# Kernel tuning notes

Hardware: AMD Instinct MI355X
Metric: run time of the kernel (lower is better)

Reference implementation:

```python
import jax, jax.numpy as jnp
import numpy as np


def setup_inputs() -> dict:
    key = jax.random.key(0)
    k1, k2 = jax.random.split(key)
    B, N, C = 2, 1024, 64  # batch_size, block_num, out_channels
    regional_means = jax.random.normal(k1, (B, N, C), dtype=jnp.float32)
    # nn.Parameter randn then kaiming_uniform_: just use scaled random weights
    W = jax.random.normal(k2, (C, C), dtype=jnp.float32) * (1.0 / np.sqrt(C))
    return {"regional_means": regional_means, "W": W, "c": C}


def reference(regional_means, W, c):
    # regional_means: (B, N, c); W: (c, c)
    B, N, _ = regional_means.shape
    M = W @ W.T  # (c, c), PSD Mahalanobis metric
    # pairwise differences diff[b, i, j] = means[b, i] - means[b, j]  -> (B, N, N, c)
    # (original materializes this via repeat/permute; sign flip from its final
    #  permute is irrelevant since the quadratic form is even)
    diff = regional_means[:, :, None, :] - regional_means[:, None, :, :]
    # quadratic form q[b,i,j] = diff^T M diff
    q = jnp.einsum('bijc,cd,bijd->bij', diff, M, diff)
    adj = jnp.exp(-q) + jnp.eye(N, dtype=regional_means.dtype)[None, :, :]
    return adj
```

## Files before the change

kernel.cpp:

```cpp
#include <hip/hip_runtime.h>
#include <math.h>


__global__ void __launch_bounds__(256) compute_Y_kernel(
    const float* __restrict__ X, const float* __restrict__ W,
    float* __restrict__ Y, float* __restrict__ r)
{
    __shared__ float Ws[64][64];
    __shared__ float Xs[4][64];

    const int t = threadIdx.x;

    const float4* W4 = (const float4*)W;
    float4* Ws4 = (float4*)&Ws[0][0];
#pragma unroll
    for (int c = 0; c < 4; ++c) Ws4[c * 256 + t] = W4[c * 256 + t];

    const int row0 = blockIdx.x * 4;
    const int rr = t >> 6;
    const int lane = t & 63;
    Xs[rr][lane] = X[(row0 + rr) * 64 + lane];
    __syncthreads();

    float y = 0.f;
#pragma unroll
    for (int k = 0; k < 64; ++k)
        y = fmaf(Xs[rr][k], Ws[k][lane], y);

    Y[(row0 + rr) * 64 + lane] = y;

    float s = y * y;
#pragma unroll
    for (int off = 32; off > 0; off >>= 1) s += __shfl_down(s, off, 64);
    if (lane == 0) r[row0 + rr] = s;
}

__global__ void __launch_bounds__(256) adj_tile_kernel(
    const float* __restrict__ Y, const float* __restrict__ r,
    float* __restrict__ out, int N)
{
    __shared__ float Yi[64][65];
    __shared__ float Yj[64][65];

    const int b  = blockIdx.z;
    const int ib = blockIdx.y * 64;
    const int jb = blockIdx.x * 64;
    const float* __restrict__ Yb = Y + (size_t)b * N * 64;
    const float* __restrict__ rb = r + (size_t)b * N;
    const int t = threadIdx.x;

#pragma unroll
    for (int c = 0; c < 16; ++c) {
        int idx = c * 256 + t;
        int row = idx >> 6, col = idx & 63;
        Yi[row][col] = Yb[(size_t)(ib + row) * 64 + col];
        Yj[row][col] = Yb[(size_t)(jb + row) * 64 + col];
    }
    __syncthreads();

    const int tj = t & 15;
    const int ti = t >> 4;
    const int i0 = ti * 4, j0 = tj * 4;

    float acc[4][4] = {};
#pragma unroll 4
    for (int k = 0; k < 64; ++k) {
        float a0 = Yi[i0 + 0][k], a1 = Yi[i0 + 1][k],
              a2 = Yi[i0 + 2][k], a3 = Yi[i0 + 3][k];
        float b0 = Yj[j0 + 0][k], b1 = Yj[j0 + 1][k],
              b2 = Yj[j0 + 2][k], b3 = Yj[j0 + 3][k];
        acc[0][0] = fmaf(a0, b0, acc[0][0]); acc[0][1] = fmaf(a0, b1, acc[0][1]);
        acc[0][2] = fmaf(a0, b2, acc[0][2]); acc[0][3] = fmaf(a0, b3, acc[0][3]);
        acc[1][0] = fmaf(a1, b0, acc[1][0]); acc[1][1] = fmaf(a1, b1, acc[1][1]);
        acc[1][2] = fmaf(a1, b2, acc[1][2]); acc[1][3] = fmaf(a1, b3, acc[1][3]);
        acc[2][0] = fmaf(a2, b0, acc[2][0]); acc[2][1] = fmaf(a2, b1, acc[2][1]);
        acc[2][2] = fmaf(a2, b2, acc[2][2]); acc[2][3] = fmaf(a2, b3, acc[2][3]);
        acc[3][0] = fmaf(a3, b0, acc[3][0]); acc[3][1] = fmaf(a3, b1, acc[3][1]);
        acc[3][2] = fmaf(a3, b2, acc[3][2]); acc[3][3] = fmaf(a3, b3, acc[3][3]);
    }

    float ri[4], rj[4];
#pragma unroll
    for (int ii = 0; ii < 4; ++ii) ri[ii] = rb[ib + i0 + ii];
#pragma unroll
    for (int jj = 0; jj < 4; ++jj) rj[jj] = rb[jb + j0 + jj];

    const size_t base = (size_t)b * N * N;
#pragma unroll
    for (int ii = 0; ii < 4; ++ii) {
        const int gi = ib + i0 + ii;
        float4 v;
#pragma unroll
        for (int jj = 0; jj < 4; ++jj) {
            const int gj = jb + j0 + jj;
            float q = ri[ii] + rj[jj] - 2.f * acc[ii][jj];
            float val = __expf(-q);
            if (gi == gj) val += 1.f;
            (&v.x)[jj] = val;
        }
        ((float4*)(out + base + (size_t)gi * N + jb))[tj] = v;
    }
}

extern "C" void kernel_launch(void* const* d_in, const int* in_sizes, int n_in,
                              void* d_out, int out_size, void* d_ws, size_t ws_size,
                              hipStream_t stream) {
    const float* X = (const float*)d_in[0];
    const float* W = (const float*)d_in[1];
    float* out = (float*)d_out;

    const int C  = 64;
    const int BN = in_sizes[0] / C;
    const int N  = (int)(((long long)out_size * C) / in_sizes[0]);
    const int B  = BN / N;

    float* Y = (float*)d_ws;
    float* r = Y + (size_t)BN * C;

    compute_Y_kernel<<<BN / 4, 256, 0, stream>>>(X, W, Y, r);
    adj_tile_kernel<<<dim3(N / 64, N / 64, B), 256, 0, stream>>>(Y, r, out, N);
}
```

Baseline: 68.24 us.

## Fuse Y=XW projection into adjacency tile kernel, recomputing per tile

Removes the separate projection kernel and workspace round-trip. Each 64x64 output tile block now loads W and its X rows into shared memory, computes Y for the i and j blocks, takes the row norms from them, and then runs the Gram product using transposed shared layouts read as float4. Diagonal tiles reuse Yi instead of computing Yj. This drops one launch and the global-memory traffic for Y and r. In exchange every tile redundantly recomputes the projection and uses more shared memory (about 70KB per block), which limits occupancy.

```diff
diff --git a/kernel.cpp b/kernel.cpp
--- a/kernel.cpp
+++ b/kernel.cpp
@@ -2,88 +2,114 @@
 #include <math.h>
 
 
-__global__ void __launch_bounds__(256) compute_Y_kernel(
+#define PAD 68
+
+__global__ void __launch_bounds__(256, 2) adj_fused_kernel(
     const float* __restrict__ X, const float* __restrict__ W,
-    float* __restrict__ Y, float* __restrict__ r)
-{
-    __shared__ float Ws[64][64];
-    __shared__ float Xs[4][64];
-
-    const int t = threadIdx.x;
-
-    const float4* W4 = (const float4*)W;
-    float4* Ws4 = (float4*)&Ws[0][0];
-#pragma unroll
-    for (int c = 0; c < 4; ++c) Ws4[c * 256 + t] = W4[c * 256 + t];
-
-    const int row0 = blockIdx.x * 4;
-    const int rr = t >> 6;
-    const int lane = t & 63;
-    Xs[rr][lane] = X[(row0 + rr) * 64 + lane];
-    __syncthreads();
-
-    float y = 0.f;
-#pragma unroll
-    for (int k = 0; k < 64; ++k)
-        y = fmaf(Xs[rr][k], Ws[k][lane], y);
-
-    Y[(row0 + rr) * 64 + lane] = y;
-
-    float s = y * y;
-#pragma unroll
-    for (int off = 32; off > 0; off >>= 1) s += __shfl_down(s, off, 64);
-    if (lane == 0) r[row0 + rr] = s;
-}
-
-__global__ void __launch_bounds__(256) adj_tile_kernel(
-    const float* __restrict__ Y, const float* __restrict__ r,
     float* __restrict__ out, int N)
 {
-    __shared__ float Yi[64][65];
-    __shared__ float Yj[64][65];
+    __shared__ float Ws [64][PAD];
+    __shared__ float Xs [64][PAD];
+    __shared__ float Yit[64][PAD];
+    __shared__ float Yjt[64][PAD];
+    __shared__ float ris[64], rjs[64];
 
     const int b  = blockIdx.z;
     const int ib = blockIdx.y * 64;
     const int jb = blockIdx.x * 64;
-    const float* __restrict__ Yb = Y + (size_t)b * N * 64;
-    const float* __restrict__ rb = r + (size_t)b * N;
-    const int t = threadIdx.x;
+    const bool samet = (ib == jb);
+    const int t  = threadIdx.x;
+    const int tr = t >> 4;
+    const int tc = t & 15;
+    const int r0 = tr * 4, c0 = tc * 4;
 
+    const float* __restrict__ Xb = X + ((size_t)b * N) * 64;
+
+    const float4* W4  = (const float4*)W;
+    const float4* Xi4 = (const float4*)(Xb + (size_t)ib * 64);
 #pragma unroll
-    for (int c = 0; c < 16; ++c) {
+    for (int c = 0; c < 4; ++c) {
         int idx = c * 256 + t;
-        int row = idx >> 6, col = idx & 63;
-        Yi[row][col] = Yb[(size_t)(ib + row) * 64 + col];
-        Yj[row][col] = Yb[(size_t)(jb + row) * 64 + col];
+        int row = idx >> 4;
+        int col = (idx & 15) * 4;
+        *(float4*)&Ws[row][col] = W4[idx];
+        *(float4*)&Xs[row][col] = Xi4[idx];
     }
     __syncthreads();
 
-    const int tj = t & 15;
-    const int ti = t >> 4;
-    const int i0 = ti * 4, j0 = tj * 4;
+    auto computeY = [&](float (*Yt)[PAD]) {
+        float y[4][4] = {};
+#pragma unroll 4
+        for (int k4 = 0; k4 < 64; k4 += 4) {
+            float4 xv[4], wv[4];
+#pragma unroll
+            for (int rr = 0; rr < 4; ++rr) xv[rr] = *(const float4*)&Xs[r0 + rr][k4];
+#pragma unroll
+            for (int kk = 0; kk < 4; ++kk) wv[kk] = *(const float4*)&Ws[k4 + kk][c0];
+#pragma unroll
+            for (int rr = 0; rr < 4; ++rr)
+#pragma unroll
+                for (int kk = 0; kk < 4; ++kk) {
+                    float x = (&xv[rr].x)[kk];
+#pragma unroll
+                    for (int cc = 0; cc < 4; ++cc)
+                        y[rr][cc] = fmaf(x, (&wv[kk].x)[cc], y[rr][cc]);
+                }
+        }
+#pragma unroll
+        for (int cc = 0; cc < 4; ++cc)
+            *(float4*)&Yt[c0 + cc][r0] =
+                make_float4(y[0][cc], y[1][cc], y[2][cc], y[3][cc]);
+    };
 
+    computeY(Yit);
+    __syncthreads();
+
+    float (*Yjp)[PAD] = Yit;
+    if (!samet) {
+        const float4* Xj4 = (const float4*)(Xb + (size_t)jb * 64);
+#pragma unroll
+        for (int c = 0; c < 4; ++c) {
+            int idx = c * 256 + t;
+            *(float4*)&Xs[idx >> 4][(idx & 15) * 4] = Xj4[idx];
+        }
+        __syncthreads();
+        computeY(Yjt);
+        Yjp = Yjt;
+        __syncthreads();
+    }
+
+    if (t < 128) {
+        const int i = t & 63;
+        float (*Yp)[PAD] = (t < 64) ? Yit : Yjp;
+        float s = 0.f;
+#pragma unroll 8
+        for (int c = 0; c < 64; ++c) { float v = Yp[c][i]; s = fmaf(v, v, s); }
+        if (t < 64) ris[i] = s; else rjs[i] = s;
+    }
+    __syncthreads();
+
+    const int i0 = r0, j0 = c0;
     float acc[4][4] = {};
-#pragma unroll 4
+#pragma unroll 8
     for (int k = 0; k < 64; ++k) {
-        float a0 = Yi[i0 + 0][k], a1 = Yi[i0 + 1][k],
-              a2 = Yi[i0 + 2][k], a3 = Yi[i0 + 3][k];
-        float b0 = Yj[j0 + 0][k], b1 = Yj[j0 + 1][k],
-              b2 = Yj[j0 + 2][k], b3 = Yj[j0 + 3][k];
-        acc[0][0] = fmaf(a0, b0, acc[0][0]); acc[0][1] = fmaf(a0, b1, acc[0][1]);
-        acc[0][2] = fmaf(a0, b2, acc[0][2]); acc[0][3] = fmaf(a0, b3, acc[0][3]);
-        acc[1][0] = fmaf(a1, b0, acc[1][0]); acc[1][1] = fmaf(a1, b1, acc[1][1]);
-        acc[1][2] = fmaf(a1, b2, acc[1][2]); acc[1][3] = fmaf(a1, b3, acc[1][3]);
-        acc[2][0] = fmaf(a2, b0, acc[2][0]); acc[2][1] = fmaf(a2, b1, acc[2][1]);
-        acc[2][2] = fmaf(a2, b2, acc[2][2]); acc[2][3] = fmaf(a2, b3, acc[2][3]);
-        acc[3][0] = fmaf(a3, b0, acc[3][0]); acc[3][1] = fmaf(a3, b1, acc[3][1]);
-        acc[3][2] = fmaf(a3, b2, acc[3][2]); acc[3][3] = fmaf(a3, b3, acc[3][3]);
+        float4 a  = *(const float4*)&Yit[k][i0];
+        float4 bb = *(const float4*)&Yjp[k][j0];
+        acc[0][0] = fmaf(a.x, bb.x, acc[0][0]); acc[0][1] = fmaf(a.x, bb.y, acc[0][1]);
+        acc[0][2] = fmaf(a.x, bb.z, acc[0][2]); acc[0][3] = fmaf(a.x, bb.w, acc[0][3]);
+        acc[1][0] = fmaf(a.y, bb.x, acc[1][0]); acc[1][1] = fmaf(a.y, bb.y, acc[1][1]);
+        acc[1][2] = fmaf(a.y, bb.z, acc[1][2]); acc[1][3] = fmaf(a.y, bb.w, acc[1][3]);
+        acc[2][0] = fmaf(a.z, bb.x, acc[2][0]); acc[2][1] = fmaf(a.z, bb.y, acc[2][1]);
+        acc[2][2] = fmaf(a.z, bb.z, acc[2][2]); acc[2][3] = fmaf(a.z, bb.w, acc[2][3]);
+        acc[3][0] = fmaf(a.w, bb.x, acc[3][0]); acc[3][1] = fmaf(a.w, bb.y, acc[3][1]);
+        acc[3][2] = fmaf(a.w, bb.z, acc[3][2]); acc[3][3] = fmaf(a.w, bb.w, acc[3][3]);
     }
 
     float ri[4], rj[4];
 #pragma unroll
-    for (int ii = 0; ii < 4; ++ii) ri[ii] = rb[ib + i0 + ii];
+    for (int ii = 0; ii < 4; ++ii) ri[ii] = ris[i0 + ii];
 #pragma unroll
-    for (int jj = 0; jj < 4; ++jj) rj[jj] = rb[jb + j0 + jj];
+    for (int jj = 0; jj < 4; ++jj) rj[jj] = rjs[j0 + jj];
 
     const size_t base = (size_t)b * N * N;
 #pragma unroll
@@ -98,7 +124,7 @@
             if (gi == gj) val += 1.f;
             (&v.x)[jj] = val;
         }
-        ((float4*)(out + base + (size_t)gi * N + jb))[tj] = v;
+        ((float4*)(out + base + (size_t)gi * N + jb))[tc] = v;
     }
 }
 
@@ -114,9 +140,5 @@
     const int N  = (int)(((long long)out_size * C) / in_sizes[0]);
     const int B  = BN / N;
 
-    float* Y = (float*)d_ws;
-    float* r = Y + (size_t)BN * C;
-
-    compute_Y_kernel<<<BN / 4, 256, 0, stream>>>(X, W, Y, r);
-    adj_tile_kernel<<<dim3(N / 64, N / 64, B), 256, 0, stream>>>(Y, r, out, N);
+    adj_fused_kernel<<<dim3(N / 64, N / 64, B), 256, 0, stream>>>(X, W, out, N);
 }
```

Result: slower. 72.54 us (+6.3%).

## Compute Gram matrix with bf16 MFMA per-wave 16x16 tiles instead of FP32 FMA

Applied to the files above, without the earlier changes.

Stores the projected Y in bf16 and computes each 16x16 block of the pairwise Gram matrix with two 16x16x32 bf16 MFMA instructions per wave, reading operands straight from global memory with no shared-memory staging. The squared norms are taken from the bf16-rounded values so they stay consistent with the dot products. The goal is to remove the FP32 FMA inner loop and the LDS tile loads. In exchange, Y loses precision, which can noticeably perturb exp(-q) for large norms. Output stores become scalar and strided per lane rather than float4 writes.

```diff
diff --git a/kernel.cpp b/kernel.cpp
--- a/kernel.cpp
+++ b/kernel.cpp
@@ -1,16 +1,19 @@
 #include <hip/hip_runtime.h>
+#include <hip/hip_bf16.h>
 #include <math.h>
 
 
-__global__ void __launch_bounds__(256) compute_Y_kernel(
+typedef __attribute__((ext_vector_type(8))) short bf16x8;
+typedef __attribute__((ext_vector_type(4))) float f32x4;
+
+__global__ void __launch_bounds__(256) y_kernel(
     const float* __restrict__ X, const float* __restrict__ W,
-    float* __restrict__ Y, float* __restrict__ r)
+    __hip_bfloat16* __restrict__ Y, float* __restrict__ r)
 {
     __shared__ float Ws[64][64];
     __shared__ float Xs[4][64];
 
     const int t = threadIdx.x;
-
     const float4* W4 = (const float4*)W;
     float4* Ws4 = (float4*)&Ws[0][0];
 #pragma unroll
@@ -19,7 +22,7 @@
     const int row0 = blockIdx.x * 4;
     const int rr = t >> 6;
     const int lane = t & 63;
-    Xs[rr][lane] = X[(row0 + rr) * 64 + lane];
+    Xs[rr][lane] = X[(size_t)(row0 + rr) * 64 + lane];
     __syncthreads();
 
     float y = 0.f;
@@ -27,78 +30,54 @@
     for (int k = 0; k < 64; ++k)
         y = fmaf(Xs[rr][k], Ws[k][lane], y);
 
-    Y[(row0 + rr) * 64 + lane] = y;
+    const __hip_bfloat16 yb = __float2bfloat16(y);
+    Y[(size_t)(row0 + rr) * 64 + lane] = yb;
 
-    float s = y * y;
+    const float yf = __bfloat162float(yb);
+    float s = yf * yf;
 #pragma unroll
     for (int off = 32; off > 0; off >>= 1) s += __shfl_down(s, off, 64);
     if (lane == 0) r[row0 + rr] = s;
 }
 
-__global__ void __launch_bounds__(256) adj_tile_kernel(
-    const float* __restrict__ Y, const float* __restrict__ r,
+__global__ void __launch_bounds__(256) gram_kernel(
+    const __hip_bfloat16* __restrict__ Y, const float* __restrict__ r,
     float* __restrict__ out, int N)
 {
-    __shared__ float Yi[64][65];
-    __shared__ float Yj[64][65];
+    const int t = threadIdx.x;
+    const int wave = t >> 6, lane = t & 63;
+    const int tpr = N >> 4;
+    const int tile = blockIdx.x * 4 + wave;
+    const int it = tile / tpr, jt = tile % tpr;
+    const int b  = blockIdx.z;
 
-    const int b  = blockIdx.z;
-    const int ib = blockIdx.y * 64;
-    const int jb = blockIdx.x * 64;
-    const float* __restrict__ Yb = Y + (size_t)b * N * 64;
-    const float* __restrict__ rb = r + (size_t)b * N;
-    const int t = threadIdx.x;
+    const int ib = it << 4, jb = jt << 4;
+    const unsigned short* Yb = (const unsigned short*)Y + (size_t)b * N * 64;
+    const float* rb = r + (size_t)b * N;
 
+    const int m  = lane & 15;
+    const int k0 = (lane >> 4) * 8;
+
+    const bf16x8 a0 = *(const bf16x8*)(Yb + (size_t)(ib + m) * 64 + k0);
+    const bf16x8 a1 = *(const bf16x8*)(Yb + (size_t)(ib + m) * 64 + k0 + 32);
+    const bf16x8 b0 = *(const bf16x8*)(Yb + (size_t)(jb + m) * 64 + k0);
+    const bf16x8 b1 = *(const bf16x8*)(Yb + (size_t)(jb + m) * 64 + k0 + 32);
+
+    f32x4 acc = {0.f, 0.f, 0.f, 0.f};
+    acc = __builtin_amdgcn_mfma_f32_16x16x32_bf16(a0, b0, acc, 0, 0, 0);
+    acc = __builtin_amdgcn_mfma_f32_16x16x32_bf16(a1, b1, acc, 0, 0, 0);
+
+    const int gj = jb + m;
+    const float rjv = rb[gj];
+    const size_t obase = (size_t)b * N * N;
+    const int quad4 = (lane >> 4) * 4;
 #pragma unroll
-    for (int c = 0; c < 16; ++c) {
-        int idx = c * 256 + t;
-        int row = idx >> 6, col = idx & 63;
-        Yi[row][col] = Yb[(size_t)(ib + row) * 64 + col];
-        Yj[row][col] = Yb[(size_t)(jb + row) * 64 + col];
-    }
-    __syncthreads();
-
-    const int tj = t & 15;
-    const int ti = t >> 4;
-    const int i0 = ti * 4, j0 = tj * 4;
-
-    float acc[4][4] = {};
-#pragma unroll 4
-    for (int k = 0; k < 64; ++k) {
-        float a0 = Yi[i0 + 0][k], a1 = Yi[i0 + 1][k],
-              a2 = Yi[i0 + 2][k], a3 = Yi[i0 + 3][k];
-        float b0 = Yj[j0 + 0][k], b1 = Yj[j0 + 1][k],
-              b2 = Yj[j0 + 2][k], b3 = Yj[j0 + 3][k];
-        acc[0][0] = fmaf(a0, b0, acc[0][0]); acc[0][1] = fmaf(a0, b1, acc[0][1]);
-        acc[0][2] = fmaf(a0, b2, acc[0][2]); acc[0][3] = fmaf(a0, b3, acc[0][3]);
-        acc[1][0] = fmaf(a1, b0, acc[1][0]); acc[1][1] = fmaf(a1, b1, acc[1][1]);
-        acc[1][2] = fmaf(a1, b2, acc[1][2]); acc[1][3] = fmaf(a1, b3, acc[1][3]);
-        acc[2][0] = fmaf(a2, b0, acc[2][0]); acc[2][1] = fmaf(a2, b1, acc[2][1]);
-        acc[2][2] = fmaf(a2, b2, acc[2][2]); acc[2][3] = fmaf(a2, b3, acc[2][3]);
-        acc[3][0] = fmaf(a3, b0, acc[3][0]); acc[3][1] = fmaf(a3, b1, acc[3][1]);
-        acc[3][2] = fmaf(a3, b2, acc[3][2]); acc[3][3] = fmaf(a3, b3, acc[3][3]);
-    }
-
-    float ri[4], rj[4];
-#pragma unroll
-    for (int ii = 0; ii < 4; ++ii) ri[ii] = rb[ib + i0 + ii];
-#pragma unroll
-    for (int jj = 0; jj < 4; ++jj) rj[jj] = rb[jb + j0 + jj];
-
-    const size_t base = (size_t)b * N * N;
-#pragma unroll
-    for (int ii = 0; ii < 4; ++ii) {
-        const int gi = ib + i0 + ii;
-        float4 v;
-#pragma unroll
-        for (int jj = 0; jj < 4; ++jj) {
-            const int gj = jb + j0 + jj;
-            float q = ri[ii] + rj[jj] - 2.f * acc[ii][jj];
-            float val = __expf(-q);
-            if (gi == gj) val += 1.f;
-            (&v.x)[jj] = val;
-        }
-        ((float4*)(out + base + (size_t)gi * N + jb))[tj] = v;
+    for (int v = 0; v < 4; ++v) {
+        const int gi = ib + quad4 + v;
+        float q = rb[gi] + rjv - 2.f * acc[v];
+        float val = __expf(-q);
+        if (gi == gj) val += 1.f;
+        out[obase + (size_t)gi * N + gj] = val;
     }
 }
 
@@ -114,9 +93,11 @@
     const int N  = (int)(((long long)out_size * C) / in_sizes[0]);
     const int B  = BN / N;
 
-    float* Y = (float*)d_ws;
-    float* r = Y + (size_t)BN * C;
+    __hip_bfloat16* Ybf = (__hip_bfloat16*)d_ws;
+    float* r = (float*)((char*)d_ws + (size_t)BN * C * sizeof(__hip_bfloat16));
 
-    compute_Y_kernel<<<BN / 4, 256, 0, stream>>>(X, W, Y, r);
-    adj_tile_kernel<<<dim3(N / 64, N / 64, B), 256, 0, stream>>>(Y, r, out, N);
+    y_kernel<<<BN / 4, 256, 0, stream>>>(X, W, Ybf, r);
+
+    const int tpr = N >> 4;
+    gram_kernel<<<dim3((tpr * tpr) / 4, 1, B), 256, 0, stream>>>(Ybf, r, out, N);
 }
```

New measurement: 66.17 us. 1.03x faster.
